# Performance work log

Hardware: AMD Instinct MI355X
Metric: run time of the kernel (lower is better)

## Reference

```python
import jax, jax.numpy as jnp
import numpy as np

SWIGLU_ALPHA = 1.702
SWIGLU_LIMIT = 7.0
B, S, H, E, K, I = 2, 2048, 2048, 32, 4, 1024


def setup_inputs() -> dict:
    key = jax.random.key(0)
    ks = jax.random.split(key, 8)
    return {
        "hidden_states": jax.random.normal(ks[0], (B, S, H), jnp.float32),
        "gate_w": jax.random.normal(ks[1], (E, H), jnp.float32) * 0.02,
        "gate_b": jnp.zeros((E,), jnp.float32),
        "w_gate": jax.random.normal(ks[2], (E, H, I), jnp.float32) * 0.02,
        "b_gate": jnp.zeros((E, I), jnp.float32),
        "w_up": jax.random.normal(ks[3], (E, H, I), jnp.float32) * 0.02,
        "b_up": jnp.zeros((E, I), jnp.float32),
        "w_down": jax.random.normal(ks[4], (E, I, H), jnp.float32) * 0.02,
        "b_down": jnp.zeros((E, H), jnp.float32),
    }


def reference(hidden_states, gate_w, gate_b, w_gate, b_gate, w_up, b_up, w_down, b_down):
    Bb, Ss, Hh = hidden_states.shape
    x = hidden_states.reshape(-1, Hh)                      # [T, H]
    # --- gate: top-k logits first, then softmax over the selected subset ---
    logits = x @ gate_w.T + gate_b                         # [T, E]
    topk_logits, topk_idx = jax.lax.top_k(logits, K)       # sorted descending
    topk_weight = jax.nn.softmax(topk_logits.astype(jnp.float32), axis=-1)  # [T, K]
    # --- dispatch: replicate each token K times, sort by expert id ---
    flat_idx = topk_idx.reshape(-1)                        # [T*K]
    xs = jnp.repeat(x, K, axis=0)                          # [T*K, H]
    order = jnp.argsort(flat_idx)                          # stable sort by expert
    xt = xs[order]
    gid = flat_idx[order]                                  # expert id per sorted row
    group_sizes = jnp.bincount(flat_idx, length=E).astype(jnp.int32)
    # --- grouped GEMM experts with GPT-OSS SwiGLU ---
    gate = jax.lax.ragged_dot(xt, w_gate, group_sizes) + b_gate[gid]
    up = jax.lax.ragged_dot(xt, w_up, group_sizes) + b_up[gid]
    gate = jnp.minimum(gate, SWIGLU_LIMIT)
    up = jnp.clip(up, -SWIGLU_LIMIT, SWIGLU_LIMIT)
    glu = gate * jax.nn.sigmoid(SWIGLU_ALPHA * gate)
    activated = (up + 1.0) * glu
    outs = jax.lax.ragged_dot(activated, w_down, group_sizes) + b_down[gid]
    # --- unsort and combine with routing weights ---
    inv = jnp.argsort(order)
    outs = outs[inv].reshape(-1, K, Hh)                    # [T, K, H]
    y = jnp.sum(outs * topk_weight[..., None], axis=1).astype(x.dtype)
    return y.reshape(Bb, Ss, Hh)
```

## Files before the change

### kernel.cpp

```cpp
#include <hip/hip_runtime.h>

#define T_TOK 4096
#define E_EXP 32
#define HDIM  2048
#define IDIM  1024
#define TKROW 16384
#define BM    128
#define MAXT  160

typedef __attribute__((ext_vector_type(8))) short   short8;
typedef __attribute__((ext_vector_type(8))) __bf16  bf16x8;
typedef __attribute__((ext_vector_type(4))) float   f32x4;

typedef const __attribute__((address_space(1))) unsigned int* gas_t;
typedef __attribute__((address_space(3))) unsigned int*       las_t;

static __device__ __forceinline__ void gload16(const void* g, void* l) {
    __builtin_amdgcn_global_load_lds((gas_t)(uintptr_t)g, (las_t)(uintptr_t)l, 16, 0, 0);
}

static __device__ __forceinline__ f32x4 mfma16(short8 a, short8 b, f32x4 c) {
    return __builtin_amdgcn_mfma_f32_16x16x32_bf16(
        __builtin_bit_cast(bf16x8, a), __builtin_bit_cast(bf16x8, b), c, 0, 0, 0);
}

static __device__ __forceinline__ unsigned short f2bf(float f) {
    unsigned u = __builtin_bit_cast(unsigned, f);
    unsigned r = (u + 0x7FFFu + ((u >> 16) & 1u)) >> 16;
    return (unsigned short)r;
}
static __device__ __forceinline__ float bf2f(unsigned short u) {
    return __builtin_bit_cast(float, ((unsigned)u) << 16);
}
static __device__ __forceinline__ unsigned cvtpk(float lo, float hi) {
    unsigned r;
    asm("v_cvt_pk_bf16_f32 %0, %1, %2" : "=v"(r) : "v"(lo), "v"(hi));
    return r;
}
static __device__ __forceinline__ short8 pack8(float v0, float v1, float v2, float v3,
                                               float v4, float v5, float v6, float v7) {
    uint4 u;
    u.x = cvtpk(v0, v1); u.y = cvtpk(v2, v3);
    u.z = cvtpk(v4, v5); u.w = cvtpk(v6, v7);
    return __builtin_bit_cast(short8, u);
}

#define VM0()   asm volatile("s_waitcnt vmcnt(0)" ::: "memory")
#define BAR()   do { __builtin_amdgcn_s_barrier(); __builtin_amdgcn_sched_barrier(0); } while (0)

__global__ __launch_bounds__(256) void gating_kernel(
    const float* __restrict__ x, const float* __restrict__ gw,
    const float* __restrict__ gb, int* __restrict__ topk_idx,
    float* __restrict__ topk_w)
{
    int wave = threadIdx.x >> 6, lane = threadIdx.x & 63;
    int t = blockIdx.x * 4 + wave;
    const float* xr = x + (size_t)t * HDIM;
    float xv[32];
#pragma unroll
    for (int j = 0; j < 32; j++) xv[j] = xr[lane + 64 * j];
    float logits[E_EXP];
#pragma unroll
    for (int e = 0; e < E_EXP; e++) {
        const float* wr = gw + (size_t)e * HDIM;
        float s = 0.f;
#pragma unroll
        for (int j = 0; j < 32; j++) s = fmaf(xv[j], wr[lane + 64 * j], s);
#pragma unroll
        for (int off = 32; off; off >>= 1) s += __shfl_xor(s, off);
        logits[e] = s + gb[e];
    }
    unsigned sel = 0;
    float v[4]; int id[4];
#pragma unroll
    for (int kk = 0; kk < 4; kk++) {
        float best = -3.4e38f; int bi = 0;
#pragma unroll
        for (int e = 0; e < E_EXP; e++) {
            bool ok = ((sel >> e) & 1u) == 0u;
            bool gt = ok && (logits[e] > best);
            best = gt ? logits[e] : best;
            bi   = gt ? e : bi;
        }
        sel |= 1u << bi; v[kk] = best; id[kk] = bi;
    }
    float m0 = v[0];
    float e0 = __expf(v[0] - m0), e1 = __expf(v[1] - m0);
    float e2 = __expf(v[2] - m0), e3 = __expf(v[3] - m0);
    float inv = 1.f / (e0 + e1 + e2 + e3);
    if (lane == 0) {
        int b4 = t * 4;
        topk_idx[b4 + 0] = id[0]; topk_w[b4 + 0] = e0 * inv;
        topk_idx[b4 + 1] = id[1]; topk_w[b4 + 1] = e1 * inv;
        topk_idx[b4 + 2] = id[2]; topk_w[b4 + 2] = e2 * inv;
        topk_idx[b4 + 3] = id[3]; topk_w[b4 + 3] = e3 * inv;
    }
}

__global__ void init_kernel(int* counts, int* fill) {
    if (threadIdx.x < E_EXP) { counts[threadIdx.x] = 0; fill[threadIdx.x] = 0; }
}

__global__ void histo_kernel(const int* __restrict__ idx, int* counts) {
    int i = blockIdx.x * 256 + threadIdx.x;
    atomicAdd(&counts[idx[i]], 1);
}

__global__ void scan_tiles_kernel(const int* counts, int* offsets,
                                  int* tile_e, int* tile_r, int* ntiles) {
    if (threadIdx.x == 0) {
        int acc = 0;
        for (int e = 0; e < E_EXP; e++) { offsets[e] = acc; acc += counts[e]; }
        offsets[E_EXP] = acc;
        int nt = 0;
        for (int e = 0; e < E_EXP; e++) {
            int c = counts[e];
            for (int r = 0; r < c; r += BM) {
                tile_e[nt] = e; tile_r[nt] = offsets[e] + r; nt++;
            }
        }
        ntiles[0] = nt;
    }
}

__global__ void scatter_kernel(const int* __restrict__ idx, const int* __restrict__ offsets,
                               int* fill, int* __restrict__ pos_of, int* __restrict__ row_tok) {
    int i = blockIdx.x * 256 + threadIdx.x;
    int e = idx[i];
    int pos = offsets[e] + atomicAdd(&fill[e], 1);
    pos_of[i] = pos;
    row_tok[pos] = i >> 2;
}

__global__ __launch_bounds__(64) void gather_kernel(
    const float* __restrict__ x, const int* __restrict__ row_tok,
    unsigned short* __restrict__ xt)
{
    int r = blockIdx.x, lane = threadIdx.x;
    const f32x4* src = (const f32x4*)(x + (size_t)row_tok[r] * HDIM);
    unsigned short* dst = xt + (size_t)r * HDIM;
#pragma unroll
    for (int j = 0; j < 8; j++) {
        f32x4 f = src[lane + 64 * j];
        uint2 o;
        o.x = cvtpk(f[0], f[1]);
        o.y = cvtpk(f[2], f[3]);
        *(uint2*)(dst + 4 * (lane + 64 * j)) = o;
    }
}

__global__ __launch_bounds__(512, 4) void gemm1_kernel(
    const unsigned short* __restrict__ xt, const float* __restrict__ w_gate,
    const float* __restrict__ b_gate, const float* __restrict__ w_up,
    const float* __restrict__ b_up, const int* __restrict__ tile_e,
    const int* __restrict__ tile_r, const int* __restrict__ ntiles,
    const int* __restrict__ offsets, const int* __restrict__ counts,
    unsigned short* __restrict__ act)
{
    int flat = blockIdx.y * 8 + blockIdx.x;
    int swz = (flat & 7) * MAXT + (flat >> 3);
    int tid = swz >> 3, nb = swz & 7;
    if (tid >= ntiles[0]) return;
    int e = tile_e[tid], row0 = tile_r[tid];
    int cnt_end = offsets[e] + counts[e];
    int n0 = nb * 128;

    __shared__ unsigned short As[2][BM * 32];
    __shared__ float Bg[2][32 * 128];
    __shared__ float Bu[2][32 * 128];

    int t = threadIdx.x, lane = t & 63, w = t >> 6;
    int wr = w >> 2, wc = w & 3;
    int lrow = lane & 15;
    int kf8 = (lane >> 4) * 8;

    f32x4 accg[4][2], accu[4][2];
#pragma unroll
    for (int m = 0; m < 4; m++)
#pragma unroll
        for (int n = 0; n < 2; n++) { accg[m][n] = (f32x4)0.f; accu[m][n] = (f32x4)0.f; }

    int arow = row0 + 16 * w + (lane >> 2);
    if (arow > TKROW - 1) arow = TKROW - 1;
    const unsigned short* aSrc = xt + (size_t)arow * HDIM + (lane & 3) * 8;
    size_t eBase = (size_t)e * ((size_t)HDIM * IDIM);
    const float* gSrc = w_gate + eBase + (size_t)(4 * w + (lane >> 5)) * IDIM + n0 + (lane & 31) * 4;
    const float* uSrc = w_up   + eBase + (size_t)(4 * w + (lane >> 5)) * IDIM + n0 + (lane & 31) * 4;

#define G1_STAGE(KT, BUF) do { \
    gload16(aSrc + (size_t)(KT) * 32, (void*)&As[BUF][(16 * w) * 32]); \
    _Pragma("unroll") for (int i_ = 0; i_ < 2; i_++) { \
        size_t ko_ = (size_t)(KT) * 32 * IDIM + (size_t)(2 * i_) * IDIM; \
        gload16(gSrc + ko_, (void*)&Bg[BUF][(4 * w + 2 * i_) * 128]); \
        gload16(uSrc + ko_, (void*)&Bu[BUF][(4 * w + 2 * i_) * 128]); \
    } } while (0)

#define G1_MFMA(BUF) do { \
    const unsigned short* Ab_ = &As[BUF][0]; \
    const float* Bgb_ = &Bg[BUF][0]; const float* Bub_ = &Bu[BUF][0]; \
    short8 bgf_[2], buf_[2]; \
    _Pragma("unroll") for (int nf_ = 0; nf_ < 2; nf_++) { \
        int nc_ = wc * 32 + nf_ * 16 + lrow; \
        bgf_[nf_] = pack8(Bgb_[(kf8 + 0) * 128 + nc_], Bgb_[(kf8 + 1) * 128 + nc_], \
                          Bgb_[(kf8 + 2) * 128 + nc_], Bgb_[(kf8 + 3) * 128 + nc_], \
                          Bgb_[(kf8 + 4) * 128 + nc_], Bgb_[(kf8 + 5) * 128 + nc_], \
                          Bgb_[(kf8 + 6) * 128 + nc_], Bgb_[(kf8 + 7) * 128 + nc_]); \
        buf_[nf_] = pack8(Bub_[(kf8 + 0) * 128 + nc_], Bub_[(kf8 + 1) * 128 + nc_], \
                          Bub_[(kf8 + 2) * 128 + nc_], Bub_[(kf8 + 3) * 128 + nc_], \
                          Bub_[(kf8 + 4) * 128 + nc_], Bub_[(kf8 + 5) * 128 + nc_], \
                          Bub_[(kf8 + 6) * 128 + nc_], Bub_[(kf8 + 7) * 128 + nc_]); \
    } \
    __builtin_amdgcn_s_setprio(1); \
    _Pragma("unroll") for (int m_ = 0; m_ < 4; m_++) { \
        int rr_ = wr * 64 + m_ * 16 + lrow; \
        short8 af_ = *(const short8*)&Ab_[rr_ * 32 + kf8]; \
        _Pragma("unroll") for (int nf_ = 0; nf_ < 2; nf_++) { \
            accg[m_][nf_] = mfma16(af_, bgf_[nf_], accg[m_][nf_]); \
            accu[m_][nf_] = mfma16(af_, buf_[nf_], accu[m_][nf_]); \
        } \
    } \
    __builtin_amdgcn_s_setprio(0); } while (0)

    G1_STAGE(0, 0);
    VM0(); BAR();
    int cur = 0;
#pragma unroll 1
    for (int kt = 0; kt < 64; kt++) {
        if (kt + 1 < 64) G1_STAGE(kt + 1, cur ^ 1);
        G1_MFMA(cur);
        VM0(); BAR();
        cur ^= 1;
    }
#undef G1_STAGE
#undef G1_MFMA

#pragma unroll
    for (int nf = 0; nf < 2; nf++) {
        int col = n0 + wc * 32 + nf * 16 + lrow;
        float bgv = b_gate[e * IDIM + col];
        float buv = b_up[e * IDIM + col];
#pragma unroll
        for (int m = 0; m < 4; m++) {
            int rb = row0 + wr * 64 + m * 16 + (lane >> 4) * 4;
#pragma unroll
            for (int r = 0; r < 4; r++) {
                int grow = rb + r;
                if (grow < cnt_end) {
                    float gv = accg[m][nf][r] + bgv;
                    float uv = accu[m][nf][r] + buv;
                    gv = fminf(gv, 7.f);
                    uv = fminf(fmaxf(uv, -7.f), 7.f);
                    float glu = gv / (1.f + __expf(-1.702f * gv));
                    act[(size_t)grow * IDIM + col] = f2bf((uv + 1.f) * glu);
                }
            }
        }
    }
}

__global__ __launch_bounds__(512, 4) void gemm2_kernel(
    const unsigned short* __restrict__ actb, const float* __restrict__ w_down,
    const float* __restrict__ b_down, const int* __restrict__ tile_e,
    const int* __restrict__ tile_r, const int* __restrict__ ntiles,
    const int* __restrict__ offsets, const int* __restrict__ counts,
    unsigned short* __restrict__ outs)
{
    int flat = blockIdx.y * 8 + blockIdx.x;
    int swz = (flat & 7) * MAXT + (flat >> 3);
    int tid = swz >> 3, nb = swz & 7;
    if (tid >= ntiles[0]) return;
    int e = tile_e[tid], row0 = tile_r[tid];
    int cnt_end = offsets[e] + counts[e];
    int n0 = nb * 256;

    __shared__ unsigned short As[2][BM * 32];
    __shared__ float Bs[2][32 * 256];

    int t = threadIdx.x, lane = t & 63, w = t >> 6;
    int wr = w >> 2, wc = w & 3;
    int lrow = lane & 15;
    int kf8 = (lane >> 4) * 8;

    f32x4 acc[4][4];
#pragma unroll
    for (int m = 0; m < 4; m++)
#pragma unroll
        for (int n = 0; n < 4; n++) acc[m][n] = (f32x4)0.f;

    int arow = row0 + 16 * w + (lane >> 2);
    if (arow > TKROW - 1) arow = TKROW - 1;
    const unsigned short* aSrc = actb + (size_t)arow * IDIM + (lane & 3) * 8;
    const float* dSrc = w_down + (size_t)e * ((size_t)IDIM * HDIM)
                        + (size_t)(4 * w) * HDIM + n0 + lane * 4;

#define G2_STAGE(KT, BUF) do { \
    gload16(aSrc + (size_t)(KT) * 32, (void*)&As[BUF][(16 * w) * 32]); \
    _Pragma("unroll") for (int i_ = 0; i_ < 4; i_++) { \
        gload16(dSrc + (size_t)(KT) * 32 * HDIM + (size_t)i_ * HDIM, \
                (void*)&Bs[BUF][(4 * w + i_) * 256]); \
    } } while (0)

#define G2_MFMA(BUF) do { \
    const unsigned short* Ab_ = &As[BUF][0]; \
    const float* Bb_ = &Bs[BUF][0]; \
    short8 bf_[4]; \
    _Pragma("unroll") for (int nf_ = 0; nf_ < 4; nf_++) { \
        int nc_ = wc * 64 + nf_ * 16 + lrow; \
        bf_[nf_] = pack8(Bb_[(kf8 + 0) * 256 + nc_], Bb_[(kf8 + 1) * 256 + nc_], \
                         Bb_[(kf8 + 2) * 256 + nc_], Bb_[(kf8 + 3) * 256 + nc_], \
                         Bb_[(kf8 + 4) * 256 + nc_], Bb_[(kf8 + 5) * 256 + nc_], \
                         Bb_[(kf8 + 6) * 256 + nc_], Bb_[(kf8 + 7) * 256 + nc_]); \
    } \
    __builtin_amdgcn_s_setprio(1); \
    _Pragma("unroll") for (int m_ = 0; m_ < 4; m_++) { \
        int rr_ = wr * 64 + m_ * 16 + lrow; \
        short8 af_ = *(const short8*)&Ab_[rr_ * 32 + kf8]; \
        _Pragma("unroll") for (int nf_ = 0; nf_ < 4; nf_++) \
            acc[m_][nf_] = mfma16(af_, bf_[nf_], acc[m_][nf_]); \
    } \
    __builtin_amdgcn_s_setprio(0); } while (0)

    G2_STAGE(0, 0);
    VM0(); BAR();
    int cur = 0;
#pragma unroll 1
    for (int kt = 0; kt < 32; kt++) {
        if (kt + 1 < 32) G2_STAGE(kt + 1, cur ^ 1);
        G2_MFMA(cur);
        VM0(); BAR();
        cur ^= 1;
    }
#undef G2_STAGE
#undef G2_MFMA

#pragma unroll
    for (int nf = 0; nf < 4; nf++) {
        int col = n0 + wc * 64 + nf * 16 + lrow;
        float bdv = b_down[e * HDIM + col];
#pragma unroll
        for (int m = 0; m < 4; m++) {
            int rb = row0 + wr * 64 + m * 16 + (lane >> 4) * 4;
#pragma unroll
            for (int r = 0; r < 4; r++) {
                int grow = rb + r;
                if (grow < cnt_end)
                    outs[(size_t)grow * HDIM + col] = f2bf(acc[m][nf][r] + bdv);
            }
        }
    }
}

__global__ __launch_bounds__(256) void combine_kernel(
    const unsigned short* __restrict__ outs, const int* __restrict__ pos_of,
    const float* __restrict__ topk_w, float* __restrict__ y)
{
    int tok = blockIdx.x;
    int c0 = threadIdx.x * 8;
    float acc[8] = {0.f, 0.f, 0.f, 0.f, 0.f, 0.f, 0.f, 0.f};
#pragma unroll
    for (int k = 0; k < 4; k++) {
        int pos = pos_of[tok * 4 + k];
        float w = topk_w[tok * 4 + k];
        short8 vv = *(const short8*)(outs + (size_t)pos * HDIM + c0);
#pragma unroll
        for (int j = 0; j < 8; j++)
            acc[j] = fmaf(w, bf2f((unsigned short)vv[j]), acc[j]);
    }
    float4 o0 = make_float4(acc[0], acc[1], acc[2], acc[3]);
    float4 o1 = make_float4(acc[4], acc[5], acc[6], acc[7]);
    *(float4*)(y + (size_t)tok * HDIM + c0)     = o0;
    *(float4*)(y + (size_t)tok * HDIM + c0 + 4) = o1;
}

extern "C" void kernel_launch(void* const* d_in, const int* in_sizes, int n_in,
                              void* d_out, int out_size, void* d_ws, size_t ws_size,
                              hipStream_t stream) {
    const float* x      = (const float*)d_in[0];
    const float* gw     = (const float*)d_in[1];
    const float* gb     = (const float*)d_in[2];
    const float* w_gate = (const float*)d_in[3];
    const float* b_gate = (const float*)d_in[4];
    const float* w_up   = (const float*)d_in[5];
    const float* b_up   = (const float*)d_in[6];
    const float* w_down = (const float*)d_in[7];
    const float* b_down = (const float*)d_in[8];
    float* y = (float*)d_out;

    char* base = (char*)d_ws;
    size_t off = 0;
    int*   topk_idx = (int*)(base + off);   off += (size_t)TKROW * 4;
    float* topk_w   = (float*)(base + off); off += (size_t)TKROW * 4;
    int*   counts   = (int*)(base + off);   off += 256;
    int*   offsets  = (int*)(base + off);   off += 256;
    int*   fill     = (int*)(base + off);   off += 256;
    int*   ntiles   = (int*)(base + off);   off += 256;
    int*   tile_e   = (int*)(base + off);   off += 1024;
    int*   tile_r   = (int*)(base + off);   off += 1024;
    int*   pos_of   = (int*)(base + off);   off += (size_t)TKROW * 4;
    int*   row_tok  = (int*)(base + off);   off += (size_t)TKROW * 4;
    unsigned short* xt   = (unsigned short*)(base + off); off += (size_t)TKROW * HDIM * 2;
    unsigned short* act  = (unsigned short*)(base + off); off += (size_t)TKROW * IDIM * 2;
    unsigned short* outs = (unsigned short*)(base + off); off += (size_t)TKROW * HDIM * 2;

    init_kernel<<<1, 64, 0, stream>>>(counts, fill);
    gating_kernel<<<T_TOK / 4, 256, 0, stream>>>(x, gw, gb, topk_idx, topk_w);
    histo_kernel<<<TKROW / 256, 256, 0, stream>>>(topk_idx, counts);
    scan_tiles_kernel<<<1, 64, 0, stream>>>(counts, offsets, tile_e, tile_r, ntiles);
    scatter_kernel<<<TKROW / 256, 256, 0, stream>>>(topk_idx, offsets, fill, pos_of, row_tok);
    gather_kernel<<<TKROW, 64, 0, stream>>>(x, row_tok, xt);
    gemm1_kernel<<<dim3(8, MAXT), 512, 0, stream>>>(
        xt, w_gate, b_gate, w_up, b_up, tile_e, tile_r, ntiles, offsets, counts, act);
    gemm2_kernel<<<dim3(8, MAXT), 512, 0, stream>>>(
        act, w_down, b_down, tile_e, tile_r, ntiles, offsets, counts, outs);
    combine_kernel<<<T_TOK, 256, 0, stream>>>(outs, pos_of, topk_w, y);
}
```

Baseline: 668.4 us.

## Convert weights to bf16 in LDS with swizzled K-major layout and register-staged prefetch

Both expert GEMMs now load fp32 weight tiles into registers two steps ahead, convert them to bf16 once, and store them into a K-major, XOR-swizzled LDS layout. The MFMA loop can then read B fragments with vector LDS loads instead of eight scalar fp32 reads plus a pack per fragment. K-step grows to 64 and N-tiles shrink, so the grid doubles in the N dimension. The aim is less LDS bandwidth, fewer bank conflicts and less conversion work in the inner loop. In exchange there are more registers, the occupancy hint drops from 4 to 2, and redundant A loads rise with the narrower N tiles.

```diff
diff --git a/kernel.cpp b/kernel.cpp
--- a/kernel.cpp
+++ b/kernel.cpp
@@ -37,16 +37,10 @@
     asm("v_cvt_pk_bf16_f32 %0, %1, %2" : "=v"(r) : "v"(lo), "v"(hi));
     return r;
 }
-static __device__ __forceinline__ short8 pack8(float v0, float v1, float v2, float v3,
-                                               float v4, float v5, float v6, float v7) {
-    uint4 u;
-    u.x = cvtpk(v0, v1); u.y = cvtpk(v2, v3);
-    u.z = cvtpk(v4, v5); u.w = cvtpk(v6, v7);
-    return __builtin_bit_cast(short8, u);
-}
-
-#define VM0()   asm volatile("s_waitcnt vmcnt(0)" ::: "memory")
-#define BAR()   do { __builtin_amdgcn_s_barrier(); __builtin_amdgcn_sched_barrier(0); } while (0)
+
+#define WAITVM(N)  asm volatile("s_waitcnt vmcnt(" #N ")" ::: "memory")
+#define LGKM0()    asm volatile("s_waitcnt lgkmcnt(0)" ::: "memory")
+#define BAR()      do { __builtin_amdgcn_s_barrier(); __builtin_amdgcn_sched_barrier(0); } while (0)
 
 __global__ __launch_bounds__(256) void gating_kernel(
     const float* __restrict__ x, const float* __restrict__ gw,
@@ -149,7 +143,7 @@
     }
 }
 
-__global__ __launch_bounds__(512, 4) void gemm1_kernel(
+__global__ __launch_bounds__(512, 2) void gemm1_kernel(
     const unsigned short* __restrict__ xt, const float* __restrict__ w_gate,
     const float* __restrict__ b_gate, const float* __restrict__ w_up,
     const float* __restrict__ b_up, const int* __restrict__ tile_e,
@@ -157,86 +151,112 @@
     const int* __restrict__ offsets, const int* __restrict__ counts,
     unsigned short* __restrict__ act)
 {
-    int flat = blockIdx.y * 8 + blockIdx.x;
-    int swz = (flat & 7) * MAXT + (flat >> 3);
-    int tid = swz >> 3, nb = swz & 7;
+    int flat = blockIdx.y * 16 + blockIdx.x;
+    int swz = (flat & 7) * 320 + (flat >> 3);
+    int tid = swz >> 4, nb = swz & 15;
     if (tid >= ntiles[0]) return;
     int e = tile_e[tid], row0 = tile_r[tid];
     int cnt_end = offsets[e] + counts[e];
-    int n0 = nb * 128;
-
-    __shared__ unsigned short As[2][BM * 32];
-    __shared__ float Bg[2][32 * 128];
-    __shared__ float Bu[2][32 * 128];
+    int n0 = nb * 64;
+
+    __shared__ unsigned short As[2][BM * 64];
+    __shared__ unsigned short Bgs[2][64 * 64];
+    __shared__ unsigned short Bus[2][64 * 64];
 
     int t = threadIdx.x, lane = t & 63, w = t >> 6;
     int wr = w >> 2, wc = w & 3;
-    int lrow = lane & 15;
-    int kf8 = (lane >> 4) * 8;
-
-    f32x4 accg[4][2], accu[4][2];
-#pragma unroll
-    for (int m = 0; m < 4; m++)
-#pragma unroll
-        for (int n = 0; n < 2; n++) { accg[m][n] = (f32x4)0.f; accu[m][n] = (f32x4)0.f; }
-
-    int arow = row0 + 16 * w + (lane >> 2);
-    if (arow > TKROW - 1) arow = TKROW - 1;
-    const unsigned short* aSrc = xt + (size_t)arow * HDIM + (lane & 3) * 8;
-    size_t eBase = (size_t)e * ((size_t)HDIM * IDIM);
-    const float* gSrc = w_gate + eBase + (size_t)(4 * w + (lane >> 5)) * IDIM + n0 + (lane & 31) * 4;
-    const float* uSrc = w_up   + eBase + (size_t)(4 * w + (lane >> 5)) * IDIM + n0 + (lane & 31) * 4;
-
-#define G1_STAGE(KT, BUF) do { \
-    gload16(aSrc + (size_t)(KT) * 32, (void*)&As[BUF][(16 * w) * 32]); \
+    int lrow = lane & 15, lg8 = (lane >> 4) * 8;
+
+    f32x4 accg[4], accu[4];
+#pragma unroll
+    for (int m = 0; m < 4; m++) { accg[m] = (f32x4)0.f; accu[m] = (f32x4)0.f; }
+
+    int arow_l = lane >> 3;
+    int achunk = (lane & 7) ^ arow_l;
+    int mat = w >> 2;
+    int bn = (t & 15) * 4, bk = ((t >> 4) & 15) * 4;
+    int bxor = (t & 7) << 3;
+    const float* bp = (mat ? w_up : w_gate)
+        + (size_t)e * ((size_t)HDIM * IDIM) + (size_t)bk * IDIM + n0 + bn;
+    unsigned short* myB0 = mat ? &Bus[0][0] : &Bgs[0][0];
+    unsigned short* myB1 = mat ? &Bus[1][0] : &Bgs[1][0];
+
+    f32x4 bS0[4], bS1[4];
+
+#define G1_STAGE_A(KT, BUF) do { \
     _Pragma("unroll") for (int i_ = 0; i_ < 2; i_++) { \
-        size_t ko_ = (size_t)(KT) * 32 * IDIM + (size_t)(2 * i_) * IDIM; \
-        gload16(gSrc + ko_, (void*)&Bg[BUF][(4 * w + 2 * i_) * 128]); \
-        gload16(uSrc + ko_, (void*)&Bu[BUF][(4 * w + 2 * i_) * 128]); \
+        int ar_ = row0 + 16 * w + 8 * i_ + arow_l; \
+        if (ar_ > TKROW - 1) ar_ = TKROW - 1; \
+        gload16(xt + (size_t)ar_ * HDIM + (size_t)(KT) * 64 + achunk * 8, \
+                (void*)&As[BUF][(16 * w + 8 * i_) * 64]); \
     } } while (0)
 
-#define G1_MFMA(BUF) do { \
-    const unsigned short* Ab_ = &As[BUF][0]; \
-    const float* Bgb_ = &Bg[BUF][0]; const float* Bub_ = &Bu[BUF][0]; \
-    short8 bgf_[2], buf_[2]; \
-    _Pragma("unroll") for (int nf_ = 0; nf_ < 2; nf_++) { \
-        int nc_ = wc * 32 + nf_ * 16 + lrow; \
-        bgf_[nf_] = pack8(Bgb_[(kf8 + 0) * 128 + nc_], Bgb_[(kf8 + 1) * 128 + nc_], \
-                          Bgb_[(kf8 + 2) * 128 + nc_], Bgb_[(kf8 + 3) * 128 + nc_], \
-                          Bgb_[(kf8 + 4) * 128 + nc_], Bgb_[(kf8 + 5) * 128 + nc_], \
-                          Bgb_[(kf8 + 6) * 128 + nc_], Bgb_[(kf8 + 7) * 128 + nc_]); \
-        buf_[nf_] = pack8(Bub_[(kf8 + 0) * 128 + nc_], Bub_[(kf8 + 1) * 128 + nc_], \
-                          Bub_[(kf8 + 2) * 128 + nc_], Bub_[(kf8 + 3) * 128 + nc_], \
-                          Bub_[(kf8 + 4) * 128 + nc_], Bub_[(kf8 + 5) * 128 + nc_], \
-                          Bub_[(kf8 + 6) * 128 + nc_], Bub_[(kf8 + 7) * 128 + nc_]); \
+#define G1_LOADB(KT, DST) do { \
+    const float* gp_ = bp + (size_t)(KT) * 64 * IDIM; \
+    _Pragma("unroll") for (int i_ = 0; i_ < 4; i_++) \
+        DST[i_] = *(const f32x4*)(gp_ + (size_t)i_ * IDIM); \
+    } while (0)
+
+#define G1_WRITEB(SRC, BUFLIT) do { \
+    unsigned short* bd_ = (BUFLIT) ? myB1 : myB0; \
+    _Pragma("unroll") for (int j_ = 0; j_ < 4; j_++) { \
+        uint2 v_; \
+        v_.x = cvtpk(SRC[0][j_], SRC[1][j_]); \
+        v_.y = cvtpk(SRC[2][j_], SRC[3][j_]); \
+        *(uint2*)&bd_[(bn + j_) * 64 + (bk ^ bxor)] = v_; \
+    } } while (0)
+
+#define G1_STEP(KT, CUR, LSET, WSET) do { \
+    short8 afA_[8], bgf_[2], buf_[2]; \
+    _Pragma("unroll") for (int m_ = 0; m_ < 4; m_++) { \
+        int rr_ = wr * 64 + m_ * 16 + lrow; int rx_ = (lrow & 7) << 3; \
+        afA_[m_ * 2]     = *(const short8*)&As[CUR][rr_ * 64 + (lg8 ^ rx_)]; \
+        afA_[m_ * 2 + 1] = *(const short8*)&As[CUR][rr_ * 64 + ((32 + lg8) ^ rx_)]; \
+    } \
+    { int rb_ = wc * 16 + lrow; int bx_ = ((rb_ >> 2) & 7) << 3; \
+      bgf_[0] = *(const short8*)&Bgs[CUR][rb_ * 64 + (lg8 ^ bx_)]; \
+      bgf_[1] = *(const short8*)&Bgs[CUR][rb_ * 64 + ((32 + lg8) ^ bx_)]; \
+      buf_[0] = *(const short8*)&Bus[CUR][rb_ * 64 + (lg8 ^ bx_)]; \
+      buf_[1] = *(const short8*)&Bus[CUR][rb_ * 64 + ((32 + lg8) ^ bx_)]; } \
+    LGKM0(); \
+    BAR(); \
+    if ((KT) + 2 < 32) { G1_STAGE_A((KT) + 2, CUR); G1_LOADB((KT) + 2, LSET); } \
+    if ((KT) + 1 < 32) { \
+        if ((KT) + 2 < 32) { WAITVM(6); } else { WAITVM(0); } \
+        G1_WRITEB(WSET, (CUR) ^ 1); \
     } \
     __builtin_amdgcn_s_setprio(1); \
     _Pragma("unroll") for (int m_ = 0; m_ < 4; m_++) { \
-        int rr_ = wr * 64 + m_ * 16 + lrow; \
-        short8 af_ = *(const short8*)&Ab_[rr_ * 32 + kf8]; \
-        _Pragma("unroll") for (int nf_ = 0; nf_ < 2; nf_++) { \
-            accg[m_][nf_] = mfma16(af_, bgf_[nf_], accg[m_][nf_]); \
-            accu[m_][nf_] = mfma16(af_, buf_[nf_], accu[m_][nf_]); \
-        } \
-    } \
-    __builtin_amdgcn_s_setprio(0); } while (0)
-
-    G1_STAGE(0, 0);
-    VM0(); BAR();
-    int cur = 0;
+        accg[m_] = mfma16(afA_[m_ * 2], bgf_[0], accg[m_]); \
+        accu[m_] = mfma16(afA_[m_ * 2], buf_[0], accu[m_]); \
+    } \
+    _Pragma("unroll") for (int m_ = 0; m_ < 4; m_++) { \
+        accg[m_] = mfma16(afA_[m_ * 2 + 1], bgf_[1], accg[m_]); \
+        accu[m_] = mfma16(afA_[m_ * 2 + 1], buf_[1], accu[m_]); \
+    } \
+    __builtin_amdgcn_s_setprio(0); \
+    LGKM0(); \
+    BAR(); \
+} while (0)
+
+    G1_STAGE_A(0, 0); G1_LOADB(0, bS0);
+    G1_STAGE_A(1, 1); G1_LOADB(1, bS1);
+    WAITVM(6);
+    G1_WRITEB(bS0, 0);
+    LGKM0(); BAR();
+
 #pragma unroll 1
-    for (int kt = 0; kt < 64; kt++) {
-        if (kt + 1 < 64) G1_STAGE(kt + 1, cur ^ 1);
-        G1_MFMA(cur);
-        VM0(); BAR();
-        cur ^= 1;
-    }
-#undef G1_STAGE
-#undef G1_MFMA
-
-#pragma unroll
-    for (int nf = 0; nf < 2; nf++) {
-        int col = n0 + wc * 32 + nf * 16 + lrow;
+    for (int kt = 0; kt < 32; kt += 2) {
+        G1_STEP(kt,     0, bS0, bS1);
+        G1_STEP(kt + 1, 1, bS1, bS0);
+    }
+#undef G1_STAGE_A
+#undef G1_LOADB
+#undef G1_WRITEB
+#undef G1_STEP
+
+    {
+        int col = n0 + wc * 16 + lrow;
         float bgv = b_gate[e * IDIM + col];
         float buv = b_up[e * IDIM + col];
 #pragma unroll
@@ -246,8 +266,8 @@
             for (int r = 0; r < 4; r++) {
                 int grow = rb + r;
                 if (grow < cnt_end) {
-                    float gv = accg[m][nf][r] + bgv;
-                    float uv = accu[m][nf][r] + buv;
+                    float gv = accg[m][r] + bgv;
+                    float uv = accu[m][r] + buv;
                     gv = fminf(gv, 7.f);
                     uv = fminf(fmaxf(uv, -7.f), 7.f);
                     float glu = gv / (1.f + __expf(-1.702f * gv));
@@ -258,84 +278,115 @@
     }
 }
 
-__global__ __launch_bounds__(512, 4) void gemm2_kernel(
+__global__ __launch_bounds__(512, 2) void gemm2_kernel(
     const unsigned short* __restrict__ actb, const float* __restrict__ w_down,
     const float* __restrict__ b_down, const int* __restrict__ tile_e,
     const int* __restrict__ tile_r, const int* __restrict__ ntiles,
     const int* __restrict__ offsets, const int* __restrict__ counts,
     unsigned short* __restrict__ outs)
 {
-    int flat = blockIdx.y * 8 + blockIdx.x;
-    int swz = (flat & 7) * MAXT + (flat >> 3);
-    int tid = swz >> 3, nb = swz & 7;
+    int flat = blockIdx.y * 16 + blockIdx.x;
+    int swz = (flat & 7) * 320 + (flat >> 3);
+    int tid = swz >> 4, nb = swz & 15;
     if (tid >= ntiles[0]) return;
     int e = tile_e[tid], row0 = tile_r[tid];
     int cnt_end = offsets[e] + counts[e];
-    int n0 = nb * 256;
-
-    __shared__ unsigned short As[2][BM * 32];
-    __shared__ float Bs[2][32 * 256];
+    int n0 = nb * 128;
+
+    __shared__ unsigned short As[2][BM * 64];
+    __shared__ unsigned short Bs[2][128 * 64];
 
     int t = threadIdx.x, lane = t & 63, w = t >> 6;
     int wr = w >> 2, wc = w & 3;
-    int lrow = lane & 15;
-    int kf8 = (lane >> 4) * 8;
-
-    f32x4 acc[4][4];
+    int lrow = lane & 15, lg8 = (lane >> 4) * 8;
+
+    f32x4 acc[4][2];
 #pragma unroll
     for (int m = 0; m < 4; m++)
 #pragma unroll
-        for (int n = 0; n < 4; n++) acc[m][n] = (f32x4)0.f;
-
-    int arow = row0 + 16 * w + (lane >> 2);
-    if (arow > TKROW - 1) arow = TKROW - 1;
-    const unsigned short* aSrc = actb + (size_t)arow * IDIM + (lane & 3) * 8;
-    const float* dSrc = w_down + (size_t)e * ((size_t)IDIM * HDIM)
-                        + (size_t)(4 * w) * HDIM + n0 + lane * 4;
-
-#define G2_STAGE(KT, BUF) do { \
-    gload16(aSrc + (size_t)(KT) * 32, (void*)&As[BUF][(16 * w) * 32]); \
-    _Pragma("unroll") for (int i_ = 0; i_ < 4; i_++) { \
-        gload16(dSrc + (size_t)(KT) * 32 * HDIM + (size_t)i_ * HDIM, \
-                (void*)&Bs[BUF][(4 * w + i_) * 256]); \
+        for (int n = 0; n < 2; n++) acc[m][n] = (f32x4)0.f;
+
+    int arow_l = lane >> 3;
+    int achunk = (lane & 7) ^ arow_l;
+    int bn = (t & 31) * 4, bk = ((t >> 5) & 15) * 4;
+    int bxor = (t & 7) << 3;
+    const float* bp = w_down + (size_t)e * ((size_t)IDIM * HDIM)
+        + (size_t)bk * HDIM + n0 + bn;
+
+    f32x4 bS0[4], bS1[4];
+
+#define G2_STAGE_A(KT, BUF) do { \
+    _Pragma("unroll") for (int i_ = 0; i_ < 2; i_++) { \
+        int ar_ = row0 + 16 * w + 8 * i_ + arow_l; \
+        if (ar_ > TKROW - 1) ar_ = TKROW - 1; \
+        gload16(actb + (size_t)ar_ * IDIM + (size_t)(KT) * 64 + achunk * 8, \
+                (void*)&As[BUF][(16 * w + 8 * i_) * 64]); \
     } } while (0)
 
-#define G2_MFMA(BUF) do { \
-    const unsigned short* Ab_ = &As[BUF][0]; \
-    const float* Bb_ = &Bs[BUF][0]; \
-    short8 bf_[4]; \
-    _Pragma("unroll") for (int nf_ = 0; nf_ < 4; nf_++) { \
-        int nc_ = wc * 64 + nf_ * 16 + lrow; \
-        bf_[nf_] = pack8(Bb_[(kf8 + 0) * 256 + nc_], Bb_[(kf8 + 1) * 256 + nc_], \
-                         Bb_[(kf8 + 2) * 256 + nc_], Bb_[(kf8 + 3) * 256 + nc_], \
-                         Bb_[(kf8 + 4) * 256 + nc_], Bb_[(kf8 + 5) * 256 + nc_], \
-                         Bb_[(kf8 + 6) * 256 + nc_], Bb_[(kf8 + 7) * 256 + nc_]); \
+#define G2_LOADB(KT, DST) do { \
+    const float* gp_ = bp + (size_t)(KT) * 64 * HDIM; \
+    _Pragma("unroll") for (int i_ = 0; i_ < 4; i_++) \
+        DST[i_] = *(const f32x4*)(gp_ + (size_t)i_ * HDIM); \
+    } while (0)
+
+#define G2_WRITEB(SRC, BUFLIT) do { \
+    _Pragma("unroll") for (int j_ = 0; j_ < 4; j_++) { \
+        uint2 v_; \
+        v_.x = cvtpk(SRC[0][j_], SRC[1][j_]); \
+        v_.y = cvtpk(SRC[2][j_], SRC[3][j_]); \
+        *(uint2*)&Bs[BUFLIT][(bn + j_) * 64 + (bk ^ bxor)] = v_; \
+    } } while (0)
+
+#define G2_STEP(KT, CUR, LSET, WSET) do { \
+    short8 afA_[8], bf_[4]; \
+    _Pragma("unroll") for (int m_ = 0; m_ < 4; m_++) { \
+        int rr_ = wr * 64 + m_ * 16 + lrow; int rx_ = (lrow & 7) << 3; \
+        afA_[m_ * 2]     = *(const short8*)&As[CUR][rr_ * 64 + (lg8 ^ rx_)]; \
+        afA_[m_ * 2 + 1] = *(const short8*)&As[CUR][rr_ * 64 + ((32 + lg8) ^ rx_)]; \
+    } \
+    _Pragma("unroll") for (int n_ = 0; n_ < 2; n_++) { \
+        int rb_ = wc * 32 + n_ * 16 + lrow; int bx_ = ((rb_ >> 2) & 7) << 3; \
+        bf_[n_ * 2]     = *(const short8*)&Bs[CUR][rb_ * 64 + (lg8 ^ bx_)]; \
+        bf_[n_ * 2 + 1] = *(const short8*)&Bs[CUR][rb_ * 64 + ((32 + lg8) ^ bx_)]; \
+    } \
+    LGKM0(); \
+    BAR(); \
+    if ((KT) + 2 < 16) { G2_STAGE_A((KT) + 2, CUR); G2_LOADB((KT) + 2, LSET); } \
+    if ((KT) + 1 < 16) { \
+        if ((KT) + 2 < 16) { WAITVM(6); } else { WAITVM(0); } \
+        G2_WRITEB(WSET, (CUR) ^ 1); \
     } \
     __builtin_amdgcn_s_setprio(1); \
-    _Pragma("unroll") for (int m_ = 0; m_ < 4; m_++) { \
-        int rr_ = wr * 64 + m_ * 16 + lrow; \
-        short8 af_ = *(const short8*)&Ab_[rr_ * 32 + kf8]; \
-        _Pragma("unroll") for (int nf_ = 0; nf_ < 4; nf_++) \
-            acc[m_][nf_] = mfma16(af_, bf_[nf_], acc[m_][nf_]); \
-    } \
-    __builtin_amdgcn_s_setprio(0); } while (0)
-
-    G2_STAGE(0, 0);
-    VM0(); BAR();
-    int cur = 0;
+    _Pragma("unroll") for (int m_ = 0; m_ < 4; m_++) \
+    _Pragma("unroll") for (int n_ = 0; n_ < 2; n_++) \
+        acc[m_][n_] = mfma16(afA_[m_ * 2], bf_[n_ * 2], acc[m_][n_]); \
+    _Pragma("unroll") for (int m_ = 0; m_ < 4; m_++) \
+    _Pragma("unroll") for (int n_ = 0; n_ < 2; n_++) \
+        acc[m_][n_] = mfma16(afA_[m_ * 2 + 1], bf_[n_ * 2 + 1], acc[m_][n_]); \
+    __builtin_amdgcn_s_setprio(0); \
+    LGKM0(); \
+    BAR(); \
+} while (0)
+
+    G2_STAGE_A(0, 0); G2_LOADB(0, bS0);
+    G2_STAGE_A(1, 1); G2_LOADB(1, bS1);
+    WAITVM(6);
+    G2_WRITEB(bS0, 0);
+    LGKM0(); BAR();
+
 #pragma unroll 1
-    for (int kt = 0; kt < 32; kt++) {
-        if (kt + 1 < 32) G2_STAGE(kt + 1, cur ^ 1);
-        G2_MFMA(cur);
-        VM0(); BAR();
-        cur ^= 1;
-    }
-#undef G2_STAGE
-#undef G2_MFMA
-
-#pragma unroll
-    for (int nf = 0; nf < 4; nf++) {
-        int col = n0 + wc * 64 + nf * 16 + lrow;
+    for (int kt = 0; kt < 16; kt += 2) {
+        G2_STEP(kt,     0, bS0, bS1);
+        G2_STEP(kt + 1, 1, bS1, bS0);
+    }
+#undef G2_STAGE_A
+#undef G2_LOADB
+#undef G2_WRITEB
+#undef G2_STEP
+
+#pragma unroll
+    for (int nf = 0; nf < 2; nf++) {
+        int col = n0 + wc * 32 + nf * 16 + lrow;
         float bdv = b_down[e * HDIM + col];
 #pragma unroll
         for (int m = 0; m < 4; m++) {
@@ -408,9 +459,9 @@
     scan_tiles_kernel<<<1, 64, 0, stream>>>(counts, offsets, tile_e, tile_r, ntiles);
     scatter_kernel<<<TKROW / 256, 256, 0, stream>>>(topk_idx, offsets, fill, pos_of, row_tok);
     gather_kernel<<<TKROW, 64, 0, stream>>>(x, row_tok, xt);
-    gemm1_kernel<<<dim3(8, MAXT), 512, 0, stream>>>(
+    gemm1_kernel<<<dim3(16, MAXT), 512, 0, stream>>>(
         xt, w_gate, b_gate, w_up, b_up, tile_e, tile_r, ntiles, offsets, counts, act);
-    gemm2_kernel<<<dim3(8, MAXT), 512, 0, stream>>>(
+    gemm2_kernel<<<dim3(16, MAXT), 512, 0, stream>>>(
         act, w_down, b_down, tile_e, tile_r, ntiles, offsets, counts, outs);
     combine_kernel<<<T_TOK, 256, 0, stream>>>(outs, pos_of, topk_w, y);
 }
```

Result: slower. 1.063 ms (+59.0%).
